# Kernel optimization log

Hardware: AMD Instinct MI355X
Metric: run time of the kernel (lower is better)

Reference implementation:

```python
import jax, jax.numpy as jnp
import numpy as np

L = 4          # n_layers
HID = 64       # hidden_channels
MODES = 16     # n_modes
HEADS = 4      # n_heads
NP_SP = 500    # spatial engram patterns
NP_FR = 200    # spectral engram patterns
ED = 8         # embed_dim
WS = 4         # spatial window size
PRIME = 31.0


def setup_inputs() -> dict:
    key = jax.random.key(0)
    ks = jax.random.split(key, 20)
    B, Cin, Cout, S = 16, 3, 1, 16384
    f = lambda k, sh: jax.random.normal(k, sh, dtype=jnp.float32) * 0.05
    ch = HID // HEADS
    return {
        "x": jax.random.normal(ks[0], (B, Cin, S), dtype=jnp.float32),
        "lift_W": f(ks[1], (Cin, HID)), "lift_b": f(ks[2], (HID,)),
        "proj_W": f(ks[3], (HID, Cout)), "proj_b": f(ks[4], (Cout,)),
        "sp_emb": f(ks[5], (L, NP_SP, ED)), "sp_W": f(ks[6], (L, ED, HID)), "sp_b": f(ks[7], (L, HID)),
        "fr_emb": f(ks[8], (L, NP_FR, ED)), "fr_W": f(ks[9], (L, ED, HID * MODES)), "fr_b": f(ks[10], (L, HID * MODES)),
        "g_W1": f(ks[11], (L, 3 * HID, 64)), "g_b1": f(ks[12], (L, 64)),
        "g_W2": f(ks[13], (L, 64, 3)), "g_b2": f(ks[14], (L, 3)),
        "mhf_Wr": f(ks[15], (L, HEADS, ch, ch, MODES)),
        "mhf_Wi": f(ks[16], (L, HEADS, ch, ch, MODES)),
    }


def _spatial_engram(x, emb, W, b):
    # x: [B, C, S] -> hash each replicate-padded window of size WS -> embedding gather -> linear
    B, C, S = x.shape
    pad = WS // 2
    xp = jnp.pad(x, ((0, 0), (0, 0), (pad, pad)), mode='edge')   # [B, C, S+WS]
    sC = xp.sum(axis=1)                                          # [B, S+WS]
    # window sum over WS consecutive positions (vectorized over all seq positions)
    wsum = sC[:, 0:S] + sC[:, 1:S + 1] + sC[:, 2:S + 2] + sC[:, 3:S + 3]  # [B, S]
    idx = (wsum * PRIME).astype(jnp.int32) % NP_SP               # truncate-toward-zero like torch .long()
    idx = jnp.clip(idx, 0, NP_SP - 1)
    e = emb[idx]                                                 # [B, S, ED] gather
    out = e @ W + b                                              # [B, S, C]
    return out.transpose(0, 2, 1)                                # [B, C, S]


def _spectral_engram(x, emb, W, b):
    B, C, S = x.shape
    xf = jnp.fft.rfft(x, axis=-1)                                # [B, C, F]
    mag = jnp.abs(xf[:, :, :MODES]).mean(axis=1)                 # [B, MODES]
    idx = ((mag * 1000.0).astype(jnp.int32)).sum(axis=1) % NP_FR # [B]
    e = emb[idx]                                                 # [B, ED]
    proj = (e @ W + b).reshape(B, C, MODES)
    full = jnp.zeros((B, C, xf.shape[-1]), dtype=xf.dtype).at[:, :, :MODES].set(proj.astype(xf.dtype))
    return jnp.fft.irfft(full, n=S, axis=-1)


def _mhf_spectral_conv(x, Wr, Wi):
    # multi-head Fourier spectral conv: per-head complex channel mixing on low modes
    B, C, S = x.shape
    ch = C // HEADS
    xf = jnp.fft.rfft(x, axis=-1)                                # [B, C, F]
    xh = xf[:, :, :MODES].reshape(B, HEADS, ch, MODES)           # [B, H, ch, M]
    Wc = Wr + 1j * Wi                                            # [H, ch, ch, M]
    of = jnp.einsum('bhim,hiom->bhom', xh, Wc).reshape(B, C, MODES)
    full = jnp.zeros((B, C, xf.shape[-1]), dtype=xf.dtype).at[:, :, :MODES].set(of)
    return jnp.fft.irfft(full, n=S, axis=-1)


def _gated_fusion(sp, mh, fr, W1, b1, W2, b2):
    g = jnp.concatenate([sp.mean(-1), mh.mean(-1), fr.mean(-1)], axis=-1)  # [B, 3C]
    h = jax.nn.relu(g @ W1 + b1)
    w = jax.nn.softmax(h @ W2 + b2, axis=-1)                     # [B, 3]
    return (w[:, 0, None, None] * sp + w[:, 1, None, None] * mh + w[:, 2, None, None] * fr)


def reference(x, lift_W, lift_b, proj_W, proj_b, sp_emb, sp_W, sp_b,
              fr_emb, fr_W, fr_b, g_W1, g_b1, g_W2, g_b2, mhf_Wr, mhf_Wi):
    # lifting: [B, Cin, S] -> [B, HID, S]
    h = jnp.einsum('bcs,cd->bds', x, lift_W) + lift_b[None, :, None]
    for i in range(L):
        sp = _spatial_engram(h, sp_emb[i], sp_W[i], sp_b[i])
        mh = _mhf_spectral_conv(h, mhf_Wr[i], mhf_Wi[i])
        fr = _spectral_engram(h, fr_emb[i], fr_W[i], fr_b[i])
        h = _gated_fusion(sp, mh, fr, g_W1[i], g_b1[i], g_W2[i], g_b2[i])
        h = jax.nn.gelu(h, approximate=False)  # torch F.gelu default = exact erf
    out = jnp.einsum('bcs,cd->bds', h, proj_W) + proj_b[None, :, None]
    return out
```

## Files before the change

kernel.cpp:

```cpp
#include <hip/hip_runtime.h>
#include <math.h>

#define B_ 16
#define CIN_ 3
#define HID_ 64
#define S_ 16384
#define MODES_ 16
#define HEADS_ 4
#define CH_ 16
#define ED_ 8
#define NPSP_ 500
#define NPFR_ 200
#define LAYERS_ 4
#define RECW_ 42

__device__ __forceinline__ double gelu_exact(double v) {
    double y = v * 0.70710678118654752440;
    double t = y * y;
    double p = -1.2290555301717926e-09;
    p = fma(p, t, 1.4807192815879218e-08);
    p = fma(p, t, -1.6365838718281893e-07);
    p = fma(p, t, 1.6462114365889246e-06);
    p = fma(p, t, -1.4925650358406251e-05);
    p = fma(p, t, 1.2055332981789664e-04);
    p = fma(p, t, -8.5483270234508528e-04);
    p = fma(p, t, 5.2239776254421878e-03);
    p = fma(p, t, -2.6866170645131252e-02);
    p = fma(p, t, 1.1283791670955126e-01);
    p = fma(p, t, -3.7612638903183752e-01);
    p = fma(p, t, 1.1283791670955126e+00);
    double er = y * p;
    if (t > 0.5000001) er = erf(y);
    return 0.5 * v * (1.0 + er);
}

__device__ __constant__ double KC_[16] = {1.0, 0.99518472667219688624,
    0.98078528040323044913, 0.95694033573220886494, 0.92387953251128675613,
    0.88192126434835502971, 0.83146961230254523708, 0.77301045336273696081,
    0.70710678118654752440, 0.63439328416364549822, 0.55557023301960222474,
    0.47139673682599764856, 0.38268343236508977173, 0.29028467725446236764,
    0.19509032201612826785, 0.09801714032956060199};
__device__ __constant__ double KS_[16] = {0.0, 0.09801714032956060199,
    0.19509032201612826785, 0.29028467725446236764, 0.38268343236508977173,
    0.47139673682599764856, 0.55557023301960222474, 0.63439328416364549822,
    0.70710678118654752440, 0.77301045336273696081, 0.83146961230254523708,
    0.88192126434835502971, 0.92387953251128675613, 0.95694033573220886494,
    0.98078528040323044913, 0.99518472667219688624};

__global__ __launch_bounds__(256) void k_lift(const float* __restrict__ x,
                                              const float* __restrict__ W,
                                              const float* __restrict__ bias,
                                              float* __restrict__ h,
                                              double* __restrict__ sC) {
    int b = blockIdx.y;
    int s = blockIdx.x * 256 + threadIdx.x;
    const float* xb = x + (size_t)b * CIN_ * S_ + s;
    double x0 = (double)xb[0];
    double x1 = (double)xb[S_];
    double x2 = (double)xb[2 * S_];
    float* hb = h + (size_t)b * HID_ * S_ + s;
    double acc = 0.0;
    for (int d = 0; d < HID_; ++d) {
        double v = x0 * (double)W[d];
        v = fma(x1, (double)W[HID_ + d], v);
        v = fma(x2, (double)W[2 * HID_ + d], v);
        v += (double)bias[d];
        hb[(size_t)d * S_] = (float)v;
        acc += v;
    }
    sC[(size_t)b * S_ + s] = acc;
}

__global__ __launch_bounds__(256) void k_hash(const double* __restrict__ sC,
                                              const float* __restrict__ emb_l,
                                              int* __restrict__ idx,
                                              double* __restrict__ Eb) {
    int b = blockIdx.y;
    int s0 = blockIdx.x * 256;
    int t = threadIdx.x;
    __shared__ double sl[260];
    for (int j = t; j < 260; j += 256) {
        int p = s0 - 2 + j;
        p = p < 0 ? 0 : (p > S_ - 1 ? S_ - 1 : p);
        sl[j] = sC[(size_t)b * S_ + p];
    }
    __syncthreads();
    double wsum = ((sl[t] + sl[t + 1]) + sl[t + 2]) + sl[t + 3];
    int ti = (int)(wsum * 31.0);
    int id = ti % NPSP_;
    if (id < 0) id += NPSP_;
    idx[(size_t)b * S_ + s0 + t] = id;

    const float* er = emb_l + id * ED_;
    double ev[8];
#pragma unroll
    for (int k = 0; k < 8; k++) ev[k] = (double)er[k];

    int lane = t & 63, wv = t >> 6;
    __shared__ double red[4][8];
#pragma unroll
    for (int k = 0; k < 8; k++) {
        double v = ev[k];
        for (int off = 32; off > 0; off >>= 1) v += __shfl_down(v, off, 64);
        if (lane == 0) red[wv][k] = v;
    }
    __syncthreads();
    if (t < 8) {
        double v = red[0][t] + red[1][t] + red[2][t] + red[3][t];
        atomicAdd(&Eb[b * ED_ + t], v);
    }
}

__global__ __launch_bounds__(256, 2) void k_dft(const float* __restrict__ h,
                                                double* __restrict__ Xr,
                                                double* __restrict__ Xi) {
    int b = blockIdx.y;
    int c0 = blockIdx.x * 2;
    int t = threadIdx.x;
    const float* h0 = h + ((size_t)(b * HID_ + c0)) * S_ + t;
    const float* h1 = h0 + S_;

    double acc[64];
#pragma unroll
    for (int k = 0; k < 64; k++) acc[k] = 0.0;

    double cmv[16], smv[16];
    cmv[0] = 1.0; smv[0] = 0.0;
    cmv[1] = cospi((double)t / 8192.0);
    smv[1] = sinpi((double)t / 8192.0);
#pragma unroll
    for (int m = 2; m < 16; m++) {
        cmv[m] = cmv[m - 1] * cmv[1] - smv[m - 1] * smv[1];
        smv[m] = smv[m - 1] * cmv[1] + cmv[m - 1] * smv[1];
    }

    for (int k = 0; k < 16; k++) {
        int s = k << 8;
        double a0 = (double)h0[s];
        double b0 = (double)h0[s + 4096];
        double c0v = (double)h0[s + 8192];
        double d0 = (double)h0[s + 12288];
        double a1 = (double)h1[s];
        double b1 = (double)h1[s + 4096];
        double c1v = (double)h1[s + 8192];
        double d1 = (double)h1[s + 12288];

        double t10 = a0 + c0v, t20 = b0 + d0;
        double g00 = t10 + t20, g20 = t10 - t20;
        double ar0 = a0 - c0v, br0 = b0 - d0;
        double t11 = a1 + c1v, t21 = b1 + d1;
        double g01 = t11 + t21, g21 = t11 - t21;
        double ar1 = a1 - c1v, br1 = b1 - d1;

        acc[0] += g00;
        acc[32] += g01;
#pragma unroll
        for (int m = 1; m < 16; m++) {
            double c = cmv[m], s_ = smv[m];
            if ((m & 1) == 0) {
                double g0x = (m & 2) ? g20 : g00;
                double g1x = (m & 2) ? g21 : g01;
                acc[m]      = fma(g0x, c,  acc[m]);
                acc[16 + m] = fma(g0x, s_, acc[16 + m]);
                acc[32 + m] = fma(g1x, c,  acc[32 + m]);
                acc[48 + m] = fma(g1x, s_, acc[48 + m]);
            } else if ((m & 2) == 0) {
                acc[m]      = fma(ar0, c,  fma(-br0, s_, acc[m]));
                acc[16 + m] = fma(ar0, s_, fma( br0, c,  acc[16 + m]));
                acc[32 + m] = fma(ar1, c,  fma(-br1, s_, acc[32 + m]));
                acc[48 + m] = fma(ar1, s_, fma( br1, c,  acc[48 + m]));
            } else {
                acc[m]      = fma(ar0, c,  fma( br0, s_, acc[m]));
                acc[16 + m] = fma(ar0, s_, fma(-br0, c,  acc[16 + m]));
                acc[32 + m] = fma(ar1, c,  fma( br1, s_, acc[32 + m]));
                acc[48 + m] = fma(ar1, s_, fma(-br1, c,  acc[48 + m]));
            }
        }
#pragma unroll
        for (int m = 1; m < 16; m++) {
            double cn = cmv[m] * KC_[m] - smv[m] * KS_[m];
            double sn = smv[m] * KC_[m] + cmv[m] * KS_[m];
            cmv[m] = cn; smv[m] = sn;
        }
    }

    int lane = t & 63, wv = t >> 6;
    __shared__ double red[4][64];
#pragma unroll
    for (int k = 0; k < 64; k++) {
        double v = acc[k];
        for (int off = 32; off > 0; off >>= 1) v += __shfl_down(v, off, 64);
        if (lane == 0) red[wv][k] = v;
    }
    __syncthreads();
    if (t < 64) {
        double v = red[0][t] + red[1][t] + red[2][t] + red[3][t];
        int cc = t >> 5, im = (t >> 4) & 1, m = t & 15;
        size_t o = ((size_t)b * HID_ + c0 + cc) * MODES_ + m;
        if (im) Xi[o] = -v;
        else    Xr[o] = v;
    }
}

__global__ __launch_bounds__(256) void k_mx(const double* __restrict__ Xr,
                                            const double* __restrict__ Xi,
                                            const float* __restrict__ mWr,
                                            const float* __restrict__ mWi,
                                            double* __restrict__ MXr,
                                            double* __restrict__ MXi) {
    int hh = blockIdx.x, b = blockIdx.y, t = threadIdx.x;
    int o = t >> 4, m = t & 15;
    size_t xb = ((size_t)b * HID_ + hh * CH_) * MODES_;
    const float* wr = mWr + (size_t)hh * CH_ * CH_ * MODES_;
    const float* wi = mWi + (size_t)hh * CH_ * CH_ * MODES_;
    double aR = 0.0, aI = 0.0;
#pragma unroll 4
    for (int i = 0; i < CH_; i++) {
        double xrv = Xr[xb + i * MODES_ + m];
        double xiv = Xi[xb + i * MODES_ + m];
        double wrv = (double)wr[(i * CH_ + o) * MODES_ + m];
        double wiv = (double)wi[(i * CH_ + o) * MODES_ + m];
        aR += xrv * wrv - xiv * wiv;
        aI += xrv * wiv + xiv * wrv;
    }
    int co = hh * CH_ + o;
    MXr[(size_t)b * 1024 + co * MODES_ + m] = aR;
    MXi[(size_t)b * 1024 + co * MODES_ + m] = aI;
}

__global__ __launch_bounds__(256) void k_gate(const double* __restrict__ Xr,
                                              const double* __restrict__ Xi,
                                              const double* __restrict__ MXr,
                                              const double* __restrict__ MXi,
                                              const float* __restrict__ fr_emb_l,
                                              const float* __restrict__ fr_W_l,
                                              const float* __restrict__ fr_b_l,
                                              const double* __restrict__ Eb,
                                              const float* __restrict__ sp_W_l,
                                              const float* __restrict__ sp_b_l,
                                              const float* __restrict__ gW1,
                                              const float* __restrict__ gb1,
                                              const float* __restrict__ gW2,
                                              const float* __restrict__ gb2,
                                              double* __restrict__ RECg) {
    int b = blockIdx.x;
    int t = threadIdx.x;
    __shared__ double sP[HID_ * MODES_];
    __shared__ double gg[192], h1s[64], sww[3];
    __shared__ int magI[MODES_];
    __shared__ int fidxS;

    if (t < MODES_) {
        double acc = 0.0;
        for (int c = 0; c < HID_; c++) {
            size_t o = (size_t)b * 1024 + c * MODES_ + t;
            double re = Xr[o];
            double im = Xi[o];
            acc += sqrt(re * re + im * im);
        }
        magI[t] = (int)(acc * (1.0 / 64.0) * 1000.0);
    }
    __syncthreads();
    if (t == 0) {
        int ssum = 0;
        for (int m = 0; m < MODES_; m++) ssum += magI[m];
        int f = ssum % NPFR_;
        if (f < 0) f += NPFR_;
        fidxS = f;
    }
    __syncthreads();

    {
        const float* fe = fr_emb_l + fidxS * ED_;
        for (int u = t; u < HID_ * MODES_; u += 256) {
            double acc = 0.0;
            for (int e = 0; e < ED_; e++)
                acc += (double)fe[e] * (double)fr_W_l[e * (HID_ * MODES_) + u];
            sP[u] = acc + (double)fr_b_l[u];
        }
    }
    __syncthreads();

    if (t < 64) {
        double a = 0.0;
        for (int e = 0; e < ED_; e++)
            a += Eb[b * ED_ + e] * (double)sp_W_l[e * 64 + t];
        gg[t]       = a * (1.0 / 16384.0) + (double)sp_b_l[t];
        gg[64 + t]  = MXr[(size_t)b * 1024 + t * MODES_] * (1.0 / 16384.0);
        gg[128 + t] = sP[t * MODES_] * (1.0 / 16384.0);
    }
    __syncthreads();
    if (t < 64) {
        double a = 0.0;
        for (int k = 0; k < 192; k++) a += gg[k] * (double)gW1[k * 64 + t];
        a += (double)gb1[t];
        h1s[t] = a > 0.0 ? a : 0.0;
    }
    __syncthreads();
    if (t == 0) {
        double l[3];
        for (int j = 0; j < 3; j++) {
            double a = 0.0;
            for (int k = 0; k < 64; k++) a += h1s[k] * (double)gW2[k * 3 + j];
            l[j] = a + (double)gb2[j];
        }
        double mx = fmax(l[0], fmax(l[1], l[2]));
        double e0 = exp(l[0] - mx), e1 = exp(l[1] - mx), e2 = exp(l[2] - mx);
        double sum = e0 + e1 + e2;
        sww[0] = e0 / sum; sww[1] = e1 / sum; sww[2] = e2 / sum;
    }
    __syncthreads();

    double w0s = sww[0], w1s = sww[1], w2s = sww[2];
    double* R = RECg + (size_t)b * HID_ * RECW_;
    for (int u = t; u < HID_ * MODES_; u += 256) {
        int c = u >> 4, m = u & 15;
        double km = (m == 0 ? 1.0 : 2.0) * (1.0 / 16384.0);
        R[c * RECW_ + 2 * m]     = km * (w1s * MXr[(size_t)b * 1024 + u] + w2s * sP[u]);
        R[c * RECW_ + 2 * m + 1] = (m == 0) ? 0.0 : -(km * w1s * MXi[(size_t)b * 1024 + u]);
    }
    for (int u = t; u < 512; u += 256) {
        int e = u >> 6, c = u & 63;
        R[c * RECW_ + 32 + e] = w0s * (double)sp_W_l[u];
    }
    if (t < 64) {
        R[t * RECW_ + 40] = w0s * (double)sp_b_l[t];
        R[t * RECW_ + 41] = 0.0;
    }
}

__global__ __launch_bounds__(256) void k_recon(const int* __restrict__ idx,
                                               const float* __restrict__ sp_emb_l,
                                               const double* __restrict__ RECg,
                                               float* __restrict__ h,
                                               double* __restrict__ sC) {
    int b = blockIdx.y;
    int s1 = blockIdx.x * 256 + threadIdx.x;
    int s2 = s1 + 8192;
    int t = threadIdx.x;
    __shared__ double rec[HID_ * RECW_];
    __shared__ float semb[NPSP_ * 9];
    for (int j = t; j < HID_ * RECW_; j += 256)
        rec[j] = RECg[(size_t)b * HID_ * RECW_ + j];
    for (int j = t; j < NPSP_ * 8; j += 256) {
        int r = j >> 3, e2i = j & 7;
        semb[r * 9 + e2i] = sp_emb_l[j];
    }
    __syncthreads();

    int id1 = idx[(size_t)b * S_ + s1];
    int id2 = idx[(size_t)b * S_ + s2];
    double e1[8], e2[8];
#pragma unroll
    for (int k = 0; k < 8; k++) e1[k] = (double)semb[id1 * 9 + k];
#pragma unroll
    for (int k = 0; k < 8; k++) e2[k] = (double)semb[id2 * 9 + k];

    double cb = cospi((double)s1 / 8192.0);
    double sb = sinpi((double)s1 / 8192.0);
    double cm[16], sm[16];
    cm[0] = 1.0; sm[0] = 0.0;
    cm[1] = cb;  sm[1] = sb;
#pragma unroll
    for (int m = 2; m < 16; m++) {
        cm[m] = cm[m - 1] * cb - sm[m - 1] * sb;
        sm[m] = sm[m - 1] * cb + cm[m - 1] * sb;
    }

    float* hb = h + (size_t)b * HID_ * S_;
    double cs1 = 0.0, cs2 = 0.0;
    for (int c = 0; c < HID_; c++) {
        const double2* r2 = (const double2*)(rec + c * RECW_);
        double base = rec[c * RECW_ + 40];
        double p1 = base, p2 = base;
#pragma unroll
        for (int k = 0; k < 4; k++) {
            double2 w = r2[16 + k];
            p1 = fma(e1[2 * k], w.x, p1);
            p1 = fma(e1[2 * k + 1], w.y, p1);
            p2 = fma(e2[2 * k], w.x, p2);
            p2 = fma(e2[2 * k + 1], w.y, p2);
        }
        double vE = 0.0, vO = 0.0;
#pragma unroll
        for (int m = 0; m < 16; m += 2) {
            double2 qe = r2[m];
            double2 qo = r2[m + 1];
            vE = fma(qe.x, cm[m], vE);
            vE = fma(qe.y, sm[m], vE);
            vO = fma(qo.x, cm[m + 1], vO);
            vO = fma(qo.y, sm[m + 1], vO);
        }
        double g1 = gelu_exact(p1 + (vE + vO));
        double g2 = gelu_exact(p2 + (vE - vO));
        hb[(size_t)c * S_ + s1] = (float)g1;
        hb[(size_t)c * S_ + s2] = (float)g2;
        cs1 += g1;
        cs2 += g2;
    }
    sC[(size_t)b * S_ + s1] = cs1;
    sC[(size_t)b * S_ + s2] = cs2;
}

__global__ __launch_bounds__(256) void k_proj(const float* __restrict__ h,
                                              const float* __restrict__ pW,
                                              const float* __restrict__ pb,
                                              float* __restrict__ out) {
    int b = blockIdx.y;
    int s = blockIdx.x * 256 + threadIdx.x;
    const float* hb = h + (size_t)b * HID_ * S_ + s;
    double acc = 0.0;
    for (int d = 0; d < HID_; d++)
        acc += (double)hb[(size_t)d * S_] * (double)pW[d];
    out[(size_t)b * S_ + s] = (float)(acc + (double)pb[0]);
}

extern "C" void kernel_launch(void* const* d_in, const int* in_sizes, int n_in,
                              void* d_out, int out_size, void* d_ws, size_t ws_size,
                              hipStream_t stream) {
    const float* x      = (const float*)d_in[0];
    const float* lift_W = (const float*)d_in[1];
    const float* lift_b = (const float*)d_in[2];
    const float* proj_W = (const float*)d_in[3];
    const float* proj_b = (const float*)d_in[4];
    const float* sp_emb = (const float*)d_in[5];
    const float* sp_W   = (const float*)d_in[6];
    const float* sp_b   = (const float*)d_in[7];
    const float* fr_emb = (const float*)d_in[8];
    const float* fr_W   = (const float*)d_in[9];
    const float* fr_b   = (const float*)d_in[10];
    const float* g_W1   = (const float*)d_in[11];
    const float* g_b1   = (const float*)d_in[12];
    const float* g_W2   = (const float*)d_in[13];
    const float* g_b2   = (const float*)d_in[14];
    const float* mhf_Wr = (const float*)d_in[15];
    const float* mhf_Wi = (const float*)d_in[16];

    char* ws = (char*)d_ws;
    float* h    = (float*)ws;   ws += (size_t)B_ * HID_ * S_ * 4;
    double* sC  = (double*)ws;  ws += (size_t)B_ * S_ * 8;
    int* idx    = (int*)ws;     ws += (size_t)B_ * S_ * 4;
    double* Xr  = (double*)ws;  ws += (size_t)B_ * HID_ * MODES_ * 8;
    double* Xi  = (double*)ws;  ws += (size_t)B_ * HID_ * MODES_ * 8;
    double* MXr = (double*)ws;  ws += (size_t)B_ * HID_ * MODES_ * 8;
    double* MXi = (double*)ws;  ws += (size_t)B_ * HID_ * MODES_ * 8;
    double* REC = (double*)ws;  ws += (size_t)B_ * HID_ * RECW_ * 8;
    double* Eb  = (double*)ws;  ws += (size_t)LAYERS_ * B_ * ED_ * 8;

    hipMemsetAsync(Eb, 0, (size_t)LAYERS_ * B_ * ED_ * 8, stream);

    dim3 blk(256);
    k_lift<<<dim3(S_ / 256, B_), blk, 0, stream>>>(x, lift_W, lift_b, h, sC);

    for (int lay = 0; lay < LAYERS_; ++lay) {
        k_hash<<<dim3(S_ / 256, B_), blk, 0, stream>>>(
            sC, sp_emb + (size_t)lay * NPSP_ * ED_, idx, Eb + (size_t)lay * B_ * ED_);
        k_dft<<<dim3(HID_ / 2, B_), blk, 0, stream>>>(h, Xr, Xi);
        k_mx<<<dim3(HEADS_, B_), blk, 0, stream>>>(
            Xr, Xi,
            mhf_Wr + (size_t)lay * HEADS_ * CH_ * CH_ * MODES_,
            mhf_Wi + (size_t)lay * HEADS_ * CH_ * CH_ * MODES_,
            MXr, MXi);
        k_gate<<<dim3(B_), blk, 0, stream>>>(
            Xr, Xi, MXr, MXi,
            fr_emb + (size_t)lay * NPFR_ * ED_,
            fr_W + (size_t)lay * ED_ * HID_ * MODES_,
            fr_b + (size_t)lay * HID_ * MODES_,
            Eb + (size_t)lay * B_ * ED_,
            sp_W + (size_t)lay * ED_ * HID_,
            sp_b + (size_t)lay * HID_,
            g_W1 + (size_t)lay * 192 * 64,
            g_b1 + (size_t)lay * 64,
            g_W2 + (size_t)lay * 64 * 3,
            g_b2 + (size_t)lay * 3,
            REC);
        k_recon<<<dim3(S_ / 512, B_), blk, 0, stream>>>(
            idx, sp_emb + (size_t)lay * NPSP_ * ED_, REC, h, sC);
    }

    k_proj<<<dim3(S_ / 256, B_), blk, 0, stream>>>(h, proj_W, proj_b, (float*)d_out);
}
```

Baseline: 587.3 us.

## Fuse mode-mixing into gate kernel and split reconstruction over channel halves

Removes the separate k_mx launch by computing the per-head complex mode mixing inside k_gate from Xr/Xi staged in shared memory. It also splits k_recon across two channel halves via a z grid dimension to double block count. Each half writes a partial channel sum, and k_hash adds the two partials. This cuts one launch per layer and raises parallelism in the dominant recon kernel, at the cost of recomputing per-block trig setup and embedding loads twice, plus extra sC traffic.

```diff
diff --git a/kernel.cpp b/kernel.cpp
--- a/kernel.cpp
+++ b/kernel.cpp
@@ -51,7 +51,7 @@
                                               const float* __restrict__ W,
                                               const float* __restrict__ bias,
                                               float* __restrict__ h,
-                                              double* __restrict__ sC) {
+                                              double* __restrict__ sC2) {
     int b = blockIdx.y;
     int s = blockIdx.x * 256 + threadIdx.x;
     const float* xb = x + (size_t)b * CIN_ * S_ + s;
@@ -59,19 +59,20 @@
     double x1 = (double)xb[S_];
     double x2 = (double)xb[2 * S_];
     float* hb = h + (size_t)b * HID_ * S_ + s;
-    double acc = 0.0;
+    double accA = 0.0, accB = 0.0;
     for (int d = 0; d < HID_; ++d) {
         double v = x0 * (double)W[d];
         v = fma(x1, (double)W[HID_ + d], v);
         v = fma(x2, (double)W[2 * HID_ + d], v);
         v += (double)bias[d];
         hb[(size_t)d * S_] = (float)v;
-        acc += v;
-    }
-    sC[(size_t)b * S_ + s] = acc;
-}
-
-__global__ __launch_bounds__(256) void k_hash(const double* __restrict__ sC,
+        if (d < 32) accA += v; else accB += v;
+    }
+    sC2[(size_t)b * S_ + s] = accA;
+    sC2[(size_t)(B_ + b) * S_ + s] = accB;
+}
+
+__global__ __launch_bounds__(256) void k_hash(const double* __restrict__ sC2,
                                               const float* __restrict__ emb_l,
                                               int* __restrict__ idx,
                                               double* __restrict__ Eb) {
@@ -82,7 +83,7 @@
     for (int j = t; j < 260; j += 256) {
         int p = s0 - 2 + j;
         p = p < 0 ? 0 : (p > S_ - 1 ? S_ - 1 : p);
-        sl[j] = sC[(size_t)b * S_ + p];
+        sl[j] = sC2[(size_t)b * S_ + p] + sC2[(size_t)(B_ + b) * S_ + p];
     }
     __syncthreads();
     double wsum = ((sl[t] + sl[t + 1]) + sl[t + 2]) + sl[t + 3];
@@ -202,36 +203,10 @@
     }
 }
 
-__global__ __launch_bounds__(256) void k_mx(const double* __restrict__ Xr,
-                                            const double* __restrict__ Xi,
-                                            const float* __restrict__ mWr,
-                                            const float* __restrict__ mWi,
-                                            double* __restrict__ MXr,
-                                            double* __restrict__ MXi) {
-    int hh = blockIdx.x, b = blockIdx.y, t = threadIdx.x;
-    int o = t >> 4, m = t & 15;
-    size_t xb = ((size_t)b * HID_ + hh * CH_) * MODES_;
-    const float* wr = mWr + (size_t)hh * CH_ * CH_ * MODES_;
-    const float* wi = mWi + (size_t)hh * CH_ * CH_ * MODES_;
-    double aR = 0.0, aI = 0.0;
-#pragma unroll 4
-    for (int i = 0; i < CH_; i++) {
-        double xrv = Xr[xb + i * MODES_ + m];
-        double xiv = Xi[xb + i * MODES_ + m];
-        double wrv = (double)wr[(i * CH_ + o) * MODES_ + m];
-        double wiv = (double)wi[(i * CH_ + o) * MODES_ + m];
-        aR += xrv * wrv - xiv * wiv;
-        aI += xrv * wiv + xiv * wrv;
-    }
-    int co = hh * CH_ + o;
-    MXr[(size_t)b * 1024 + co * MODES_ + m] = aR;
-    MXi[(size_t)b * 1024 + co * MODES_ + m] = aI;
-}
-
 __global__ __launch_bounds__(256) void k_gate(const double* __restrict__ Xr,
                                               const double* __restrict__ Xi,
-                                              const double* __restrict__ MXr,
-                                              const double* __restrict__ MXi,
+                                              const float* __restrict__ mWr,
+                                              const float* __restrict__ mWi,
                                               const float* __restrict__ fr_emb_l,
                                               const float* __restrict__ fr_W_l,
                                               const float* __restrict__ fr_b_l,
@@ -245,22 +220,47 @@
                                               double* __restrict__ RECg) {
     int b = blockIdx.x;
     int t = threadIdx.x;
-    __shared__ double sP[HID_ * MODES_];
+    __shared__ double sXr[1024], sXi[1024];
+    __shared__ double sMr[1024], sMi[1024], sP[1024];
     __shared__ double gg[192], h1s[64], sww[3];
     __shared__ int magI[MODES_];
     __shared__ int fidxS;
 
+    for (int j = t; j < 1024; j += 256) {
+        sXr[j] = Xr[(size_t)b * 1024 + j];
+        sXi[j] = Xi[(size_t)b * 1024 + j];
+    }
+    __syncthreads();
+
     if (t < MODES_) {
         double acc = 0.0;
         for (int c = 0; c < HID_; c++) {
-            size_t o = (size_t)b * 1024 + c * MODES_ + t;
-            double re = Xr[o];
-            double im = Xi[o];
+            double re = sXr[c * MODES_ + t];
+            double im = sXi[c * MODES_ + t];
             acc += sqrt(re * re + im * im);
         }
         magI[t] = (int)(acc * (1.0 / 64.0) * 1000.0);
     }
-    __syncthreads();
+
+    for (int u = t; u < 1024; u += 256) {
+        int hh = u >> 8, rem = u & 255, o = rem >> 4, m = rem & 15;
+        const float* wr = mWr + (size_t)hh * CH_ * CH_ * MODES_;
+        const float* wi = mWi + (size_t)hh * CH_ * CH_ * MODES_;
+        double aR = 0.0, aI = 0.0;
+#pragma unroll 4
+        for (int i = 0; i < CH_; i++) {
+            double xrv = sXr[(hh * CH_ + i) * MODES_ + m];
+            double xiv = sXi[(hh * CH_ + i) * MODES_ + m];
+            double wrv = (double)wr[(i * CH_ + o) * MODES_ + m];
+            double wiv = (double)wi[(i * CH_ + o) * MODES_ + m];
+            aR += xrv * wrv - xiv * wiv;
+            aI += xrv * wiv + xiv * wrv;
+        }
+        sMr[(hh * CH_ + o) * MODES_ + m] = aR;
+        sMi[(hh * CH_ + o) * MODES_ + m] = aI;
+    }
+    __syncthreads();
+
     if (t == 0) {
         int ssum = 0;
         for (int m = 0; m < MODES_; m++) ssum += magI[m];
@@ -272,10 +272,10 @@
 
     {
         const float* fe = fr_emb_l + fidxS * ED_;
-        for (int u = t; u < HID_ * MODES_; u += 256) {
+        for (int u = t; u < 1024; u += 256) {
             double acc = 0.0;
             for (int e = 0; e < ED_; e++)
-                acc += (double)fe[e] * (double)fr_W_l[e * (HID_ * MODES_) + u];
+                acc += (double)fe[e] * (double)fr_W_l[e * 1024 + u];
             sP[u] = acc + (double)fr_b_l[u];
         }
     }
@@ -286,7 +286,7 @@
         for (int e = 0; e < ED_; e++)
             a += Eb[b * ED_ + e] * (double)sp_W_l[e * 64 + t];
         gg[t]       = a * (1.0 / 16384.0) + (double)sp_b_l[t];
-        gg[64 + t]  = MXr[(size_t)b * 1024 + t * MODES_] * (1.0 / 16384.0);
+        gg[64 + t]  = sMr[t * MODES_] * (1.0 / 16384.0);
         gg[128 + t] = sP[t * MODES_] * (1.0 / 16384.0);
     }
     __syncthreads();
@@ -313,11 +313,11 @@
 
     double w0s = sww[0], w1s = sww[1], w2s = sww[2];
     double* R = RECg + (size_t)b * HID_ * RECW_;
-    for (int u = t; u < HID_ * MODES_; u += 256) {
+    for (int u = t; u < 1024; u += 256) {
         int c = u >> 4, m = u & 15;
         double km = (m == 0 ? 1.0 : 2.0) * (1.0 / 16384.0);
-        R[c * RECW_ + 2 * m]     = km * (w1s * MXr[(size_t)b * 1024 + u] + w2s * sP[u]);
-        R[c * RECW_ + 2 * m + 1] = (m == 0) ? 0.0 : -(km * w1s * MXi[(size_t)b * 1024 + u]);
+        R[c * RECW_ + 2 * m]     = km * (w1s * sMr[u] + w2s * sP[u]);
+        R[c * RECW_ + 2 * m + 1] = (m == 0) ? 0.0 : -(km * w1s * sMi[u]);
     }
     for (int u = t; u < 512; u += 256) {
         int e = u >> 6, c = u & 63;
@@ -333,15 +333,17 @@
                                                const float* __restrict__ sp_emb_l,
                                                const double* __restrict__ RECg,
                                                float* __restrict__ h,
-                                               double* __restrict__ sC) {
+                                               double* __restrict__ sC2) {
     int b = blockIdx.y;
+    int cz = blockIdx.z;
+    int cbase = cz * 32;
     int s1 = blockIdx.x * 256 + threadIdx.x;
     int s2 = s1 + 8192;
     int t = threadIdx.x;
-    __shared__ double rec[HID_ * RECW_];
+    __shared__ double rec[32 * RECW_];
     __shared__ float semb[NPSP_ * 9];
-    for (int j = t; j < HID_ * RECW_; j += 256)
-        rec[j] = RECg[(size_t)b * HID_ * RECW_ + j];
+    for (int j = t; j < 32 * RECW_; j += 256)
+        rec[j] = RECg[(size_t)b * HID_ * RECW_ + cbase * RECW_ + j];
     for (int j = t; j < NPSP_ * 8; j += 256) {
         int r = j >> 3, e2i = j & 7;
         semb[r * 9 + e2i] = sp_emb_l[j];
@@ -367,9 +369,9 @@
         sm[m] = sm[m - 1] * cb + cm[m - 1] * sb;
     }
 
-    float* hb = h + (size_t)b * HID_ * S_;
+    float* hb = h + (size_t)b * HID_ * S_ + (size_t)cbase * S_;
     double cs1 = 0.0, cs2 = 0.0;
-    for (int c = 0; c < HID_; c++) {
+    for (int c = 0; c < 32; c++) {
         const double2* r2 = (const double2*)(rec + c * RECW_);
         double base = rec[c * RECW_ + 40];
         double p1 = base, p2 = base;
@@ -398,8 +400,8 @@
         cs1 += g1;
         cs2 += g2;
     }
-    sC[(size_t)b * S_ + s1] = cs1;
-    sC[(size_t)b * S_ + s2] = cs2;
+    sC2[(size_t)(cz * B_ + b) * S_ + s1] = cs1;
+    sC2[(size_t)(cz * B_ + b) * S_ + s2] = cs2;
 }
 
 __global__ __launch_bounds__(256) void k_proj(const float* __restrict__ h,
@@ -438,31 +440,26 @@
 
     char* ws = (char*)d_ws;
     float* h    = (float*)ws;   ws += (size_t)B_ * HID_ * S_ * 4;
-    double* sC  = (double*)ws;  ws += (size_t)B_ * S_ * 8;
+    double* sC2 = (double*)ws;  ws += (size_t)2 * B_ * S_ * 8;
     int* idx    = (int*)ws;     ws += (size_t)B_ * S_ * 4;
     double* Xr  = (double*)ws;  ws += (size_t)B_ * HID_ * MODES_ * 8;
     double* Xi  = (double*)ws;  ws += (size_t)B_ * HID_ * MODES_ * 8;
-    double* MXr = (double*)ws;  ws += (size_t)B_ * HID_ * MODES_ * 8;
-    double* MXi = (double*)ws;  ws += (size_t)B_ * HID_ * MODES_ * 8;
     double* REC = (double*)ws;  ws += (size_t)B_ * HID_ * RECW_ * 8;
     double* Eb  = (double*)ws;  ws += (size_t)LAYERS_ * B_ * ED_ * 8;
 
     hipMemsetAsync(Eb, 0, (size_t)LAYERS_ * B_ * ED_ * 8, stream);
 
     dim3 blk(256);
-    k_lift<<<dim3(S_ / 256, B_), blk, 0, stream>>>(x, lift_W, lift_b, h, sC);
+    k_lift<<<dim3(S_ / 256, B_), blk, 0, stream>>>(x, lift_W, lift_b, h, sC2);
 
     for (int lay = 0; lay < LAYERS_; ++lay) {
         k_hash<<<dim3(S_ / 256, B_), blk, 0, stream>>>(
-            sC, sp_emb + (size_t)lay * NPSP_ * ED_, idx, Eb + (size_t)lay * B_ * ED_);
+            sC2, sp_emb + (size_t)lay * NPSP_ * ED_, idx, Eb + (size_t)lay * B_ * ED_);
         k_dft<<<dim3(HID_ / 2, B_), blk, 0, stream>>>(h, Xr, Xi);
-        k_mx<<<dim3(HEADS_, B_), blk, 0, stream>>>(
+        k_gate<<<dim3(B_), blk, 0, stream>>>(
             Xr, Xi,
             mhf_Wr + (size_t)lay * HEADS_ * CH_ * CH_ * MODES_,
             mhf_Wi + (size_t)lay * HEADS_ * CH_ * CH_ * MODES_,
-            MXr, MXi);
-        k_gate<<<dim3(B_), blk, 0, stream>>>(
-            Xr, Xi, MXr, MXi,
             fr_emb + (size_t)lay * NPFR_ * ED_,
             fr_W + (size_t)lay * ED_ * HID_ * MODES_,
             fr_b + (size_t)lay * HID_ * MODES_,
@@ -474,8 +471,8 @@
             g_W2 + (size_t)lay * 64 * 3,
             g_b2 + (size_t)lay * 3,
             REC);
-        k_recon<<<dim3(S_ / 512, B_), blk, 0, stream>>>(
-            idx, sp_emb + (size_t)lay * NPSP_ * ED_, REC, h, sC);
+        k_recon<<<dim3(S_ / 512, B_, 2), blk, 0, stream>>>(
+            idx, sp_emb + (size_t)lay * NPSP_ * ED_, REC, h, sC2);
     }
 
     k_proj<<<dim3(S_ / 256, B_), blk, 0, stream>>>(h, proj_W, proj_b, (float*)d_out);
```

New measurement: 595.6 us. Within noise of the previous version (+1.4%).
